# Performance work log

Hardware: AMD Instinct MI355X
Metric: run time of the kernel (lower is better)

Reference implementation:

```python
import jax, jax.numpy as jnp
import numpy as np

N = 100000          # nodes
E = 1600000         # edges (avg degree 16)
IN_DIM = 64
HID = 64
OUT = 32
NUM_GRAPHS = 64


def setup_inputs() -> dict:
    key = jax.random.key(0)
    ks = jax.random.split(key, 12)
    x = jax.random.normal(ks[0], (N, IN_DIM), dtype=jnp.float32)
    edge_index = jax.random.randint(ks[1], (2, E), 0, N, dtype=jnp.int64)
    batch = jnp.sort(jax.random.randint(ks[2], (N,), 0, NUM_GRAPHS, dtype=jnp.int64))
    s = 0.05
    return {
        "x": x,
        "edge_index": edge_index,
        "batch": batch,
        "w1_init": jax.random.normal(ks[3], (IN_DIM, HID), dtype=jnp.float32) * s,
        "w1_root": jax.random.normal(ks[4], (IN_DIM, HID), dtype=jnp.float32) * s,
        "b1": jnp.zeros((HID,), dtype=jnp.float32),
        "w2_init": jax.random.normal(ks[5], (HID, HID), dtype=jnp.float32) * s,
        "w2_root": jax.random.normal(ks[6], (HID, HID), dtype=jnp.float32) * s,
        "b2": jnp.zeros((HID,), dtype=jnp.float32),
        "fc_w": jax.random.normal(ks[7], (HID, OUT), dtype=jnp.float32) * s,
        "fc_b": jnp.zeros((OUT,), dtype=jnp.float32),
    }


def reference(x, edge_index, batch, w1_init, w1_root, b1, w2_init, w2_root, b2, fc_w, fc_b):
    row, col = edge_index[0], edge_index[1]
    # gcn_norm without self loops (ARMAConv default): deg over target nodes
    ones_e = jnp.ones((E,), dtype=x.dtype)
    deg = jax.ops.segment_sum(ones_e, col, num_segments=N)
    dinv = jnp.where(deg > 0, jax.lax.rsqrt(jnp.maximum(deg, 1.0)), 0.0)
    norm = dinv[row] * dinv[col]  # [E]

    def propagate(h):  # out[col] += norm * h[row]
        return jax.ops.segment_sum(h[row] * norm[:, None], col, num_segments=N)

    # ARMAConv (K=1, T=1, act=None): A_hat (x W_init) + x W_root + b
    h = jax.nn.relu(propagate(x @ w1_init) + x @ w1_root + b1)
    h = jax.nn.relu(propagate(h @ w2_init) + h @ w2_root + b2)

    # global mean pool over graphs
    cnt = jax.ops.segment_sum(jnp.ones((N,), dtype=h.dtype), batch, num_segments=NUM_GRAPHS)
    pooled = jax.ops.segment_sum(h, batch, num_segments=NUM_GRAPHS) / jnp.maximum(cnt, 1.0)[:, None]

    return pooled @ fc_w + fc_b  # [NUM_GRAPHS, OUT]
```

## Files before the change

### kernel.cpp

```cpp
#include <hip/hip_runtime.h>
#include <hip/hip_bf16.h>


#define NB 256
#define CAP 5120
#define MAXB 400
#define P1_CHUNK 2048

typedef unsigned int uint32;
typedef unsigned short ushort16;
typedef __attribute__((ext_vector_type(8))) short short8;
typedef __attribute__((ext_vector_type(4))) float f32x4;

__device__ inline uint32 bf16rn(float f) {
    uint32 u = __float_as_uint(f);
    uint32 r = ((u >> 16) & 1u) + 0x7FFFu;
    return (u + r) >> 16;
}
__device__ inline uint32 pack_bf16(float a, float b) {
    return bf16rn(a) | (bf16rn(b) << 16);
}
__device__ inline float bflo(uint32 u) { return __uint_as_float(u << 16); }
__device__ inline float bfhi(uint32 u) { return __uint_as_float(u & 0xFFFF0000u); }

__global__ __launch_bounds__(256) void bucket_kernel(
    const int* __restrict__ row, const int* __restrict__ col,
    uint32* __restrict__ bpack, int* __restrict__ bcnt, int E) {
    __shared__ int hist[MAXB];
    __shared__ int ofs[MAXB];
    __shared__ int cur[MAXB];
    __shared__ int gbase[MAXB];
    __shared__ int s[256];
    __shared__ uint32 stage[P1_CHUNK];
    __shared__ unsigned short stage_bk[P1_CHUNK];

    int t = threadIdx.x;
    for (int i = t; i < MAXB; i += 256) hist[i] = 0;
    __syncthreads();

    int e0 = blockIdx.x * P1_CHUNK;
    int cntE = min(E - e0, P1_CHUNK);

    for (int i = t; i < cntE; i += 256) {
        int c = col[e0 + i];
        atomicAdd(&hist[c >> 8], 1);
    }
    __syncthreads();

    int i2 = 2 * t;
    int a = (i2 < MAXB) ? hist[i2] : 0;
    int b = (i2 + 1 < MAXB) ? hist[i2 + 1] : 0;
    s[t] = a + b;
    __syncthreads();
    for (int off = 1; off < 256; off <<= 1) {
        int x = (t >= off) ? s[t - off] : 0;
        __syncthreads();
        s[t] += x;
        __syncthreads();
    }
    int excl = (t > 0) ? s[t - 1] : 0;
    if (i2 < MAXB) ofs[i2] = excl;
    if (i2 + 1 < MAXB) ofs[i2 + 1] = excl + a;
    __syncthreads();

    for (int i = t; i < MAXB; i += 256) {
        cur[i] = ofs[i];
        gbase[i] = hist[i] ? atomicAdd(&bcnt[i], hist[i]) : 0;
    }
    __syncthreads();

    for (int i = t; i < cntE; i += 256) {
        int c = col[e0 + i];
        int r = row[e0 + i];
        int bk = c >> 8;
        int k = atomicAdd(&cur[bk], 1);
        stage[k] = ((uint32)(c & 255) << 24) | (uint32)r;
        stage_bk[k] = (unsigned short)bk;
    }
    __syncthreads();

    for (int i = t; i < cntE; i += 256) {
        uint32 pk = stage[i];
        int bk = stage_bk[i];
        int gd = gbase[bk] + (i - ofs[bk]);
        if (gd < CAP) bpack[(size_t)bk * CAP + gd] = pk;
    }
}

__global__ __launch_bounds__(1024) void csr_kernel(
    const uint32* __restrict__ bpack, const int* __restrict__ bcnt,
    int* __restrict__ es, int* __restrict__ nstart, int* __restrict__ ndeg,
    float* __restrict__ dinv, int n) {
    __shared__ uint32 sbp[CAP];
    __shared__ int h[NB];
    __shared__ int s[NB];
    __shared__ int cur[NB];
    int b = blockIdx.x, t = threadIdx.x;
    if (t < NB) h[t] = 0;
    __syncthreads();
    int cnt = min(bcnt[b], CAP);
    size_t base = (size_t)b * CAP;
    for (int i = t; i < cnt; i += 1024) {
        uint32 pk = bpack[base + i];
        sbp[i] = pk;
        atomicAdd(&h[pk >> 24], 1);
    }
    __syncthreads();
    if (t < NB) s[t] = h[t];
    __syncthreads();
    for (int off = 1; off < NB; off <<= 1) {
        int x = 0;
        if (t < NB && t >= off) x = s[t - off];
        __syncthreads();
        if (t < NB) s[t] += x;
        __syncthreads();
    }
    if (t < NB) {
        int myofs = s[t] - h[t];
        cur[t] = myofs;
        int node = b * NB + t;
        if (node < n) {
            nstart[node] = (int)base + myofs;
            ndeg[node] = h[t];
            dinv[node] = h[t] ? rsqrtf((float)h[t]) : 0.0f;
        }
    }
    __syncthreads();
    for (int i = t; i < cnt; i += 1024) {
        uint32 pk = sbp[i];
        int cl = (int)(pk >> 24);
        int p = atomicAdd(&cur[cl], 1);
        es[base + p] = (int)(pk & 0xFFFFFFu);
    }
}

__global__ __launch_bounds__(256) void wprep_kernel(
    const float* __restrict__ W1i, const float* __restrict__ W1r,
    const float* __restrict__ W2i, const float* __restrict__ W2r,
    ushort16* __restrict__ wt) {
    int idx = blockIdx.x * 256 + threadIdx.x;
    if (idx >= 8 * 4096) return;
    int m = idx >> 12;
    int r = idx & 4095;
    int d = r >> 6, k = r & 63;
    const float* W = (m < 2) ? W1i : (m < 4) ? W1r : (m < 6) ? W2i : W2r;
    float v = W[k * 64 + d];
    uint32 hi = bf16rn(v);
    uint32 outv;
    if (m & 1) {
        float hf = __uint_as_float(hi << 16);
        outv = bf16rn(v - hf);
    } else {
        outv = hi;
    }
    wt[(size_t)m * 4096 + d * 64 + k] = (unsigned short)outv;
}

__global__ __launch_bounds__(256) void gemm_mfma(
    const void* __restrict__ Xin,
    const ushort16* __restrict__ wt4,
    const float* __restrict__ bias, const float* __restrict__ dinv,
    ushort16* __restrict__ Ts, ushort16* __restrict__ Rs, int n, int xf32) {
    __shared__ unsigned short sXs[64 * 72];
    int t = threadIdx.x;
    int node0 = blockIdx.x * 64;

    if (xf32) {
        const float* X = (const float*)Xin;
        for (int i = t; i < 1024; i += 256) {
            int r = i >> 4, c4 = (i & 15) * 4;
            int node = node0 + r;
            float4 v = make_float4(0.f, 0.f, 0.f, 0.f);
            if (node < n) v = *(const float4*)&X[(size_t)node * 64 + c4];
            *(uint32*)&sXs[r * 72 + c4] = pack_bf16(v.x, v.y);
            *(uint32*)&sXs[r * 72 + c4 + 2] = pack_bf16(v.z, v.w);
        }
    } else {
        const uint32* Xb2 = (const uint32*)Xin;
        for (int i = t; i < 512; i += 256) {
            int r = i >> 3, kg = i & 7;
            int node = node0 + r;
            uint4 v = make_uint4(0u, 0u, 0u, 0u);
            if (node < n) v = *(const uint4*)&Xb2[(size_t)node * 32 + kg * 4];
            *(uint4*)&sXs[r * 72 + kg * 8] = v;
        }
    }

    int w = t >> 6;
    int lane = t & 63;
    int q = lane >> 4;
    int col = lane & 15;
    int dim = w * 16 + col;

    short8 bih[2], bil[2], brh[2], brl[2];
#pragma unroll
    for (int kh = 0; kh < 2; ++kh) {
        size_t o = (size_t)dim * 64 + kh * 32 + q * 8;
        bih[kh] = *(const short8*)&wt4[0 * 4096 + o];
        bil[kh] = *(const short8*)&wt4[1 * 4096 + o];
        brh[kh] = *(const short8*)&wt4[2 * 4096 + o];
        brl[kh] = *(const short8*)&wt4[3 * 4096 + o];
    }
    float bi = bias[dim];
    __syncthreads();

#pragma unroll
    for (int mt = 0; mt < 4; ++mt) {
        int rbase = mt * 16 + col;
        short8 a0 = *(const short8*)&sXs[rbase * 72 + q * 8];
        short8 a1 = *(const short8*)&sXs[rbase * 72 + 32 + q * 8];
        f32x4 accT = {0.f, 0.f, 0.f, 0.f};
        f32x4 accR = {0.f, 0.f, 0.f, 0.f};
        accT = __builtin_amdgcn_mfma_f32_16x16x32_bf16(a0, bih[0], accT, 0, 0, 0);
        accT = __builtin_amdgcn_mfma_f32_16x16x32_bf16(a1, bih[1], accT, 0, 0, 0);
        accT = __builtin_amdgcn_mfma_f32_16x16x32_bf16(a0, bil[0], accT, 0, 0, 0);
        accT = __builtin_amdgcn_mfma_f32_16x16x32_bf16(a1, bil[1], accT, 0, 0, 0);
        accR = __builtin_amdgcn_mfma_f32_16x16x32_bf16(a0, brh[0], accR, 0, 0, 0);
        accR = __builtin_amdgcn_mfma_f32_16x16x32_bf16(a1, brh[1], accR, 0, 0, 0);
        accR = __builtin_amdgcn_mfma_f32_16x16x32_bf16(a0, brl[0], accR, 0, 0, 0);
        accR = __builtin_amdgcn_mfma_f32_16x16x32_bf16(a1, brl[1], accR, 0, 0, 0);
#pragma unroll
        for (int reg = 0; reg < 4; ++reg) {
            int node = node0 + mt * 16 + q * 4 + reg;
            if (node < n) {
                float dv = dinv[node];
                Ts[(size_t)node * 64 + dim] = (unsigned short)bf16rn(accT[reg] * dv);
                Rs[(size_t)node * 64 + dim] = (unsigned short)bf16rn(accR[reg] + bi);
            }
        }
    }
}

__global__ __launch_bounds__(256) void gather_fused(
    const uint2* __restrict__ Ts2, const uint2* __restrict__ Rs2,
    const int* __restrict__ es, const int* __restrict__ nstart,
    const int* __restrict__ ndeg, const float* __restrict__ dinv,
    uint2* __restrict__ Hb2, int n) {
    int c = blockIdx.x * 4 + (threadIdx.x >> 6);
    if (c >= n) return;
    int lane = threadIdx.x & 63;
    int q = lane >> 4;
    int d4 = lane & 15;
    int deg = ndeg[c];
    int s0 = nstart[c];
    float a0 = 0.f, a1 = 0.f, a2 = 0.f, a3 = 0.f;
    for (int base = 0; base < deg; base += 64) {
        int m = min(deg - base, 64);
        int sid = (lane < m) ? es[s0 + base + lane] : 0;
        for (int j = 0; j < m; j += 16) {
            int e0 = j + q, e1 = j + 4 + q, e2 = j + 8 + q, e3 = j + 12 + q;
            int r0 = __shfl(sid, e0);
            int r1 = __shfl(sid, e1);
            int r2 = __shfl(sid, e2);
            int r3 = __shfl(sid, e3);
            uint2 z = make_uint2(0u, 0u);
            uint2 v0 = (e0 < m) ? Ts2[(size_t)r0 * 16 + d4] : z;
            uint2 v1 = (e1 < m) ? Ts2[(size_t)r1 * 16 + d4] : z;
            uint2 v2 = (e2 < m) ? Ts2[(size_t)r2 * 16 + d4] : z;
            uint2 v3 = (e3 < m) ? Ts2[(size_t)r3 * 16 + d4] : z;
            a0 += bflo(v0.x) + bflo(v1.x) + bflo(v2.x) + bflo(v3.x);
            a1 += bfhi(v0.x) + bfhi(v1.x) + bfhi(v2.x) + bfhi(v3.x);
            a2 += bflo(v0.y) + bflo(v1.y) + bflo(v2.y) + bflo(v3.y);
            a3 += bfhi(v0.y) + bfhi(v1.y) + bfhi(v2.y) + bfhi(v3.y);
        }
    }
    a0 += __shfl_xor(a0, 16); a0 += __shfl_xor(a0, 32);
    a1 += __shfl_xor(a1, 16); a1 += __shfl_xor(a1, 32);
    a2 += __shfl_xor(a2, 16); a2 += __shfl_xor(a2, 32);
    a3 += __shfl_xor(a3, 16); a3 += __shfl_xor(a3, 32);
    if (lane < 16) {
        float dc = dinv[c];
        uint2 ur = Rs2[(size_t)c * 16 + d4];
        float h0 = fmaxf(fmaf(dc, a0, bflo(ur.x)), 0.0f);
        float h1 = fmaxf(fmaf(dc, a1, bfhi(ur.x)), 0.0f);
        float h2 = fmaxf(fmaf(dc, a2, bflo(ur.y)), 0.0f);
        float h3 = fmaxf(fmaf(dc, a3, bfhi(ur.y)), 0.0f);
        Hb2[(size_t)c * 16 + d4] = make_uint2(pack_bf16(h0, h1), pack_bf16(h2, h3));
    }
}

__global__ __launch_bounds__(256) void pool_kernel(
    const uint32* __restrict__ Hb, const int* __restrict__ batch,
    float* __restrict__ pooled, float* __restrict__ cnt, int n) {
    __shared__ float sAcc[64 * 64];
    __shared__ float sCnt[64];
    int tid = threadIdx.x;
    for (int i = tid; i < 4096; i += 256) sAcc[i] = 0.0f;
    if (tid < 64) sCnt[tid] = 0.0f;
    __syncthreads();

    int w = tid >> 6, lane = tid & 63;
    int half = lane >> 5, d2 = lane & 31;
    int s = blockIdx.x * 256 + w * 64;
    int e = min(s + 64, n);
    float a0 = 0.0f, a1 = 0.0f, c = 0.0f;
    int gcur = -1;
    for (int i = s + half; i < e; i += 2) {
        int g = batch[i];
        if (g != gcur) {
            if (gcur >= 0) {
                atomicAdd(&sAcc[gcur * 64 + 2 * d2], a0);
                atomicAdd(&sAcc[gcur * 64 + 2 * d2 + 1], a1);
                if (d2 == 0) atomicAdd(&sCnt[gcur], c);
            }
            gcur = g; a0 = 0.0f; a1 = 0.0f; c = 0.0f;
        }
        uint32 u = Hb[(size_t)i * 32 + d2];
        a0 += bflo(u);
        a1 += bfhi(u);
        c += 1.0f;
    }
    if (gcur >= 0) {
        atomicAdd(&sAcc[gcur * 64 + 2 * d2], a0);
        atomicAdd(&sAcc[gcur * 64 + 2 * d2 + 1], a1);
        if (d2 == 0) atomicAdd(&sCnt[gcur], c);
    }
    __syncthreads();
    for (int i = tid; i < 4096; i += 256) {
        float v = sAcc[i];
        if (v != 0.0f) atomicAdd(&pooled[i], v);
    }
    if (tid < 64) {
        float v = sCnt[tid];
        if (v != 0.0f) atomicAdd(&cnt[tid], v);
    }
}

__global__ void final_fc(const float* __restrict__ pooled, const float* __restrict__ cnt,
                         const float* __restrict__ fcw, const float* __restrict__ fcb,
                         float* __restrict__ out) {
    int idx = blockIdx.x * 256 + threadIdx.x;
    if (idx >= 64 * 32) return;
    int g = idx >> 5, o = idx & 31;
    float c = fmaxf(cnt[g], 1.0f);
    float acc = 0.0f;
#pragma unroll
    for (int k = 0; k < 64; ++k) acc = fmaf(pooled[g * 64 + k], fcw[k * 32 + o], acc);
    out[idx] = acc / c + fcb[o];
}

extern "C" void kernel_launch(void* const* d_in, const int* in_sizes, int n_in,
                              void* d_out, int out_size, void* d_ws, size_t ws_size,
                              hipStream_t stream) {
    const float* x       = (const float*)d_in[0];
    const int*   eidx    = (const int*)d_in[1];
    const int*   batch   = (const int*)d_in[2];
    const float* w1_init = (const float*)d_in[3];
    const float* w1_root = (const float*)d_in[4];
    const float* b1      = (const float*)d_in[5];
    const float* w2_init = (const float*)d_in[6];
    const float* w2_root = (const float*)d_in[7];
    const float* b2      = (const float*)d_in[8];
    const float* fc_w    = (const float*)d_in[9];
    const float* fc_b    = (const float*)d_in[10];
    float* out = (float*)d_out;

    const int N = in_sizes[0] / 64;
    const int E = in_sizes[1] / 2;
    const int* row = eidx;
    const int* col = eidx + E;

    const int B = (N + NB - 1) / NB;

    uint32* bpack = (uint32*)d_ws;
    int*   es     = (int*)(bpack + (size_t)B * CAP);
    int*   bcnt   = es + (size_t)B * CAP;
    float* pooled = (float*)(bcnt + MAXB);
    float* cnt    = pooled + 64 * 64;
    int*   nstart = (int*)(cnt + 64);
    int*   ndeg   = nstart + N;
    float* dinv   = (float*)(ndeg + N);
    uint32* wtU   = (uint32*)(dinv + N);
    uint32* Ts    = wtU + 16384;
    uint32* Rs    = Ts + (size_t)N * 32;
    uint32* Hb    = Rs + (size_t)N * 32;
    ushort16* wt  = (ushort16*)wtU;

    hipMemsetAsync(bcnt, 0, (size_t)(MAXB + 64 * 64 + 64) * sizeof(int), stream);

    wprep_kernel<<<(8 * 4096 + 255) / 256, 256, 0, stream>>>(w1_init, w1_root, w2_init, w2_root, wt);
    bucket_kernel<<<(E + P1_CHUNK - 1) / P1_CHUNK, 256, 0, stream>>>(row, col, bpack, bcnt, E);
    csr_kernel<<<B, 1024, 0, stream>>>(bpack, bcnt, es, nstart, ndeg, dinv, N);

    gemm_mfma<<<(N + 63) / 64, 256, 0, stream>>>(x, wt, b1, dinv,
                                                 (ushort16*)Ts, (ushort16*)Rs, N, 1);
    gather_fused<<<(N + 3) / 4, 256, 0, stream>>>((const uint2*)Ts, (const uint2*)Rs,
                                                  es, nstart, ndeg, dinv, (uint2*)Hb, N);

    gemm_mfma<<<(N + 63) / 64, 256, 0, stream>>>(Hb, wt + (size_t)4 * 4096, b2, dinv,
                                                 (ushort16*)Ts, (ushort16*)Rs, N, 0);
    gather_fused<<<(N + 3) / 4, 256, 0, stream>>>((const uint2*)Ts, (const uint2*)Rs,
                                                  es, nstart, ndeg, dinv, (uint2*)Hb, N);

    pool_kernel<<<(N + 255) / 256, 256, 0, stream>>>(Hb, batch, pooled, cnt, N);
    final_fc<<<(64 * 32 + 255) / 256, 256, 0, stream>>>(pooled, cnt, fc_w, fc_b, out);
}
```

Measured before the change: 293.7 us.

## Fuse weight prep into bucket kernel, vectorize GEMM stores, nontemporal edge loads

```diff
diff --git a/kernel.cpp b/kernel.cpp
--- a/kernel.cpp
+++ b/kernel.cpp
@@ -25,7 +25,10 @@
 
 __global__ __launch_bounds__(256) void bucket_kernel(
     const int* __restrict__ row, const int* __restrict__ col,
-    uint32* __restrict__ bpack, int* __restrict__ bcnt, int E) {
+    uint32* __restrict__ bpack, int* __restrict__ bcnt, int E,
+    const float* __restrict__ W1i, const float* __restrict__ W1r,
+    const float* __restrict__ W2i, const float* __restrict__ W2r,
+    ushort16* __restrict__ wt) {
     __shared__ int hist[MAXB];
     __shared__ int ofs[MAXB];
     __shared__ int cur[MAXB];
@@ -35,10 +38,30 @@
     __shared__ unsigned short stage_bk[P1_CHUNK];
 
     int t = threadIdx.x;
+
+    if (blockIdx.x < 128) {
+        int idx = blockIdx.x * 256 + t;
+        int m = idx >> 12;
+        int r = idx & 4095;
+        int d = r >> 6, k = r & 63;
+        const float* W = (m < 2) ? W1i : (m < 4) ? W1r : (m < 6) ? W2i : W2r;
+        float v = W[k * 64 + d];
+        uint32 hi = bf16rn(v);
+        uint32 outv;
+        if (m & 1) {
+            float hf = __uint_as_float(hi << 16);
+            outv = bf16rn(v - hf);
+        } else {
+            outv = hi;
+        }
+        wt[(size_t)m * 4096 + d * 64 + k] = (unsigned short)outv;
+        return;
+    }
+
     for (int i = t; i < MAXB; i += 256) hist[i] = 0;
     __syncthreads();
 
-    int e0 = blockIdx.x * P1_CHUNK;
+    int e0 = (blockIdx.x - 128) * P1_CHUNK;
     int cntE = min(E - e0, P1_CHUNK);
 
     for (int i = t; i < cntE; i += 256) {
@@ -134,28 +157,6 @@
     }
 }
 
-__global__ __launch_bounds__(256) void wprep_kernel(
-    const float* __restrict__ W1i, const float* __restrict__ W1r,
-    const float* __restrict__ W2i, const float* __restrict__ W2r,
-    ushort16* __restrict__ wt) {
-    int idx = blockIdx.x * 256 + threadIdx.x;
-    if (idx >= 8 * 4096) return;
-    int m = idx >> 12;
-    int r = idx & 4095;
-    int d = r >> 6, k = r & 63;
-    const float* W = (m < 2) ? W1i : (m < 4) ? W1r : (m < 6) ? W2i : W2r;
-    float v = W[k * 64 + d];
-    uint32 hi = bf16rn(v);
-    uint32 outv;
-    if (m & 1) {
-        float hf = __uint_as_float(hi << 16);
-        outv = bf16rn(v - hf);
-    } else {
-        outv = hi;
-    }
-    wt[(size_t)m * 4096 + d * 64 + k] = (unsigned short)outv;
-}
-
 __global__ __launch_bounds__(256) void gemm_mfma(
     const void* __restrict__ Xin,
     const ushort16* __restrict__ wt4,
@@ -201,8 +202,11 @@
         brh[kh] = *(const short8*)&wt4[2 * 4096 + o];
         brl[kh] = *(const short8*)&wt4[3 * 4096 + o];
     }
-    float bi = bias[dim];
-    __syncthreads();
+    float4 bias4 = *(const float4*)&bias[w * 16 + q * 4];
+    __syncthreads();
+
+    unsigned short* TsU = (unsigned short*)Ts;
+    unsigned short* RsU = (unsigned short*)Rs;
 
 #pragma unroll
     for (int mt = 0; mt < 4; ++mt) {
@@ -211,22 +215,26 @@
         short8 a1 = *(const short8*)&sXs[rbase * 72 + 32 + q * 8];
         f32x4 accT = {0.f, 0.f, 0.f, 0.f};
         f32x4 accR = {0.f, 0.f, 0.f, 0.f};
-        accT = __builtin_amdgcn_mfma_f32_16x16x32_bf16(a0, bih[0], accT, 0, 0, 0);
-        accT = __builtin_amdgcn_mfma_f32_16x16x32_bf16(a1, bih[1], accT, 0, 0, 0);
-        accT = __builtin_amdgcn_mfma_f32_16x16x32_bf16(a0, bil[0], accT, 0, 0, 0);
-        accT = __builtin_amdgcn_mfma_f32_16x16x32_bf16(a1, bil[1], accT, 0, 0, 0);
-        accR = __builtin_amdgcn_mfma_f32_16x16x32_bf16(a0, brh[0], accR, 0, 0, 0);
-        accR = __builtin_amdgcn_mfma_f32_16x16x32_bf16(a1, brh[1], accR, 0, 0, 0);
-        accR = __builtin_amdgcn_mfma_f32_16x16x32_bf16(a0, brl[0], accR, 0, 0, 0);
-        accR = __builtin_amdgcn_mfma_f32_16x16x32_bf16(a1, brl[1], accR, 0, 0, 0);
-#pragma unroll
-        for (int reg = 0; reg < 4; ++reg) {
-            int node = node0 + mt * 16 + q * 4 + reg;
-            if (node < n) {
-                float dv = dinv[node];
-                Ts[(size_t)node * 64 + dim] = (unsigned short)bf16rn(accT[reg] * dv);
-                Rs[(size_t)node * 64 + dim] = (unsigned short)bf16rn(accR[reg] + bi);
-            }
+        accT = __builtin_amdgcn_mfma_f32_16x16x32_bf16(bih[0], a0, accT, 0, 0, 0);
+        accT = __builtin_amdgcn_mfma_f32_16x16x32_bf16(bih[1], a1, accT, 0, 0, 0);
+        accT = __builtin_amdgcn_mfma_f32_16x16x32_bf16(bil[0], a0, accT, 0, 0, 0);
+        accT = __builtin_amdgcn_mfma_f32_16x16x32_bf16(bil[1], a1, accT, 0, 0, 0);
+        accR = __builtin_amdgcn_mfma_f32_16x16x32_bf16(brh[0], a0, accR, 0, 0, 0);
+        accR = __builtin_amdgcn_mfma_f32_16x16x32_bf16(brh[1], a1, accR, 0, 0, 0);
+        accR = __builtin_amdgcn_mfma_f32_16x16x32_bf16(brl[0], a0, accR, 0, 0, 0);
+        accR = __builtin_amdgcn_mfma_f32_16x16x32_bf16(brl[1], a1, accR, 0, 0, 0);
+
+        int node = node0 + mt * 16 + col;
+        if (node < n) {
+            float dv = dinv[node];
+            uint2 pT, pR;
+            pT.x = pack_bf16(accT[0] * dv, accT[1] * dv);
+            pT.y = pack_bf16(accT[2] * dv, accT[3] * dv);
+            pR.x = pack_bf16(accR[0] + bias4.x, accR[1] + bias4.y);
+            pR.y = pack_bf16(accR[2] + bias4.z, accR[3] + bias4.w);
+            size_t o = (size_t)node * 64 + w * 16 + q * 4;
+            *(uint2*)&TsU[o] = pT;
+            *(uint2*)&RsU[o] = pR;
         }
     }
 }
@@ -246,7 +254,7 @@
     float a0 = 0.f, a1 = 0.f, a2 = 0.f, a3 = 0.f;
     for (int base = 0; base < deg; base += 64) {
         int m = min(deg - base, 64);
-        int sid = (lane < m) ? es[s0 + base + lane] : 0;
+        int sid = (lane < m) ? __builtin_nontemporal_load(&es[s0 + base + lane]) : 0;
         for (int j = 0; j < m; j += 16) {
             int e0 = j + q, e1 = j + 4 + q, e2 = j + 8 + q, e3 = j + 12 + q;
             int r0 = __shfl(sid, e0);
@@ -378,8 +386,9 @@
 
     hipMemsetAsync(bcnt, 0, (size_t)(MAXB + 64 * 64 + 64) * sizeof(int), stream);
 
-    wprep_kernel<<<(8 * 4096 + 255) / 256, 256, 0, stream>>>(w1_init, w1_root, w2_init, w2_root, wt);
-    bucket_kernel<<<(E + P1_CHUNK - 1) / P1_CHUNK, 256, 0, stream>>>(row, col, bpack, bcnt, E);
+    const int EB = (E + P1_CHUNK - 1) / P1_CHUNK;
+    bucket_kernel<<<128 + EB, 256, 0, stream>>>(row, col, bpack, bcnt, E,
+                                                w1_init, w1_root, w2_init, w2_root, wt);
     csr_kernel<<<B, 1024, 0, stream>>>(bpack, bcnt, es, nstart, ndeg, dinv, N);
 
     gemm_mfma<<<(N + 63) / 64, 256, 0, stream>>>(x, wt, b1, dinv,
```

New measurement: 294.5 us. No clear change (+0.3%).
